# Optimization experiments

Measured on AMD Instinct MI355X. Metric: run time of the kernel, lower is better.

Reference implementation:

```python
import jax, jax.numpy as jnp
import numpy as np

B, S, D, H, L = 16, 1024, 128, 8, 3
DFF = 4 * D  # 512
DH = D // H  # 16
NUM_CLASSES = 6


def layernorm(x, g, b, eps):
    mu = jnp.mean(x, axis=-1, keepdims=True)
    var = jnp.mean(jnp.square(x - mu), axis=-1, keepdims=True)
    return g * (x - mu) / jnp.sqrt(var + eps) + b


def setup_inputs() -> dict:
    key = jax.random.key(0)
    ks = jax.random.split(key, 16)
    sc = 0.05
    inp = {
        'x': jax.random.normal(ks[0], (B, S, D), dtype=jnp.float32),
        'Wq': jax.random.normal(ks[1], (L, D, D), dtype=jnp.float32) * sc,
        'bq': jnp.zeros((L, D), dtype=jnp.float32),
        'Wk': jax.random.normal(ks[2], (L, D, D), dtype=jnp.float32) * sc,
        'bk': jnp.zeros((L, D), dtype=jnp.float32),
        'Wv': jax.random.normal(ks[3], (L, D, D), dtype=jnp.float32) * sc,
        'bv': jnp.zeros((L, D), dtype=jnp.float32),
        'ln1_g': jnp.ones((L, D), dtype=jnp.float32),
        'ln1_b': jnp.zeros((L, D), dtype=jnp.float32),
        'W1': jax.random.normal(ks[4], (L, D, DFF), dtype=jnp.float32) * sc,
        'b1': jnp.zeros((L, DFF), dtype=jnp.float32),
        'W2': jax.random.normal(ks[5], (L, DFF, D), dtype=jnp.float32) * sc,
        'b2': jnp.zeros((L, D), dtype=jnp.float32),
        'ln2_g': jnp.ones((L, D), dtype=jnp.float32),
        'ln2_b': jnp.zeros((L, D), dtype=jnp.float32),
        'Wout': jax.random.normal(ks[6], (D, NUM_CLASSES), dtype=jnp.float32) * sc,
        'bout': jnp.zeros((NUM_CLASSES,), dtype=jnp.float32),
    }
    return inp


def reference(x, Wq, bq, Wk, bk, Wv, bv, ln1_g, ln1_b, W1, b1, W2, b2, ln2_g, ln2_b, Wout, bout):
    scale = 1.0 / jnp.sqrt(jnp.float32(DH))
    for l in range(L):
        # Q/K/V projections with ReLU activation (as in source Dense(..., relu))
        q = jax.nn.relu(jnp.einsum('bsd,de->bse', x, Wq[l]) + bq[l])
        k = jax.nn.relu(jnp.einsum('bsd,de->bse', x, Wk[l]) + bk[l])
        v = jax.nn.relu(jnp.einsum('bsd,de->bse', x, Wv[l]) + bv[l])
        # split-heads (tf.split axis=-1 / concat axis=0 == reshape to heads)
        qh = q.reshape(B, S, H, DH)
        kh = k.reshape(B, S, H, DH)
        vh = v.reshape(B, S, H, DH)
        scores = jnp.einsum('bqhd,bkhd->bhqk', qh, kh) * scale  # [B,H,S,S]
        attn = jax.nn.softmax(scores, axis=-1)
        o = jnp.einsum('bhqk,bkhd->bqhd', attn, vh).reshape(B, S, D)
        x = layernorm(o + x, ln1_g[l], ln1_b[l], 1e-8)
        # pointwise FFN (Conv1D kernel_size=1 == dense over last dim)
        h = jax.nn.relu(jnp.einsum('bsd,df->bsf', x, W1[l]) + b1[l])
        f = jnp.einsum('bsf,fd->bsd', h, W2[l]) + b2[l]
        x = layernorm(f + x, ln2_g[l], ln2_b[l], 1e-6)
    return jnp.einsum('bsd,dc->bsc', x, Wout) + bout
```

## Files before the change

### kernel.cpp

```cpp
#include <hip/hip_runtime.h>
#include <math.h>

#define Bq 16
#define Sq 1024
#define Dq 128
#define Hq 8
#define DHq 16
#define DFFq 512
#define Lq 3
#define NCLS 6
#define NROWS (Bq * Sq)
#define NX ((size_t)NROWS * Dq)

#define QSCL 0.36067376022224085f

typedef __attribute__((ext_vector_type(8))) short    bf16x8;
typedef __attribute__((ext_vector_type(4))) float    f32x4;
typedef __attribute__((ext_vector_type(4))) _Float16 f16x4;
typedef __attribute__((ext_vector_type(8))) _Float16 f16x8;

__device__ inline ushort f32_to_bf16(float f) {
    union { float f; unsigned u; } v; v.f = f;
    unsigned r = v.u + 0x7fffu + ((v.u >> 16) & 1u);
    return (ushort)(r >> 16);
}

__device__ __forceinline__ float exp2_raw(float x) {
    float r;
    asm("v_exp_f32 %0, %1" : "=v"(r) : "v"(x));
    return r;
}

__global__ __launch_bounds__(256) void prep_kernel(
    const float* __restrict__ Wqp, const float* __restrict__ Wkp,
    const float* __restrict__ Wvp, const float* __restrict__ W1p,
    const float* __restrict__ W2p, const float* __restrict__ xp,
    ushort* __restrict__ wbf, ushort* __restrict__ xbf)
{
    const int gid = blockIdx.x * 256 + threadIdx.x;
    if (gid < 147456) {
        const int w   = gid / 49152;
        const int rem = gid - w * 49152;
        const int l   = rem >> 14;
        const int idx = rem & 16383;
        const int k   = idx >> 7;
        const int n   = idx & 127;
        const float* src = (w == 0) ? Wqp : (w == 1) ? Wkp : Wvp;
        const float scl = (w == 0) ? QSCL : 1.0f;
        wbf[(size_t)(w * 3 + l) * 16384 + n * 128 + k] =
            f32_to_bf16(src[(size_t)l * 16384 + k * 128 + n] * scl);
    } else if (gid < 344064) {
        const int g   = gid - 147456;
        const int l   = g >> 16;
        const int idx = g & 65535;
        const int k   = idx >> 9;
        const int n   = idx & 511;
        wbf[147456 + (size_t)l * 65536 + n * 128 + k] =
            f32_to_bf16(W1p[(size_t)l * 65536 + k * 512 + n]);
    } else if (gid < 540672) {
        const int g   = gid - 344064;
        const int l   = g >> 16;
        const int idx = g & 65535;
        const int k   = idx >> 7;
        const int n   = idx & 127;
        wbf[344064 + (size_t)l * 65536 + n * 512 + k] =
            f32_to_bf16(W2p[(size_t)l * 65536 + k * 128 + n]);
    } else {
        const int g = gid - 540672;
        xbf[g] = f32_to_bf16(xp[g]);
    }
}

__global__ __launch_bounds__(256) void gemm_qkv(
    const ushort* __restrict__ A,
    const ushort* __restrict__ wq, const ushort* __restrict__ wk,
    const ushort* __restrict__ wv,
    const float* __restrict__ bqp, const float* __restrict__ bkp,
    const float* __restrict__ bvp,
    _Float16* __restrict__ qo, _Float16* __restrict__ ko,
    _Float16* __restrict__ vo)
{
    __shared__ ushort As[64 * 40];
    __shared__ ushort Bs[128 * 40];

    const int sel  = blockIdx.y;
    const ushort* Bt   = (sel == 0) ? wq : (sel == 1) ? wk : wv;
    const float*  bias = (sel == 0) ? bqp : (sel == 1) ? bkp : bvp;
    const float   bscl = (sel == 0) ? QSCL : 1.0f;

    const int tid  = threadIdx.x;
    const int row0 = blockIdx.x * 64;
    const int wave = tid >> 6;
    const int lane = tid & 63;
    const int quad = lane >> 4;
    const int m16  = lane & 15;
    const int wm   = wave >> 1;
    const int wn   = wave & 1;

    const int sar = tid >> 2;
    const int sac = (tid & 3) * 8;

    f32x4 acc[2][4];
    #pragma unroll
    for (int i = 0; i < 2; ++i)
        #pragma unroll
        for (int j = 0; j < 4; ++j) acc[i][j] = (f32x4)0.f;

    for (int k0 = 0; k0 < 128; k0 += 32) {
        bf16x8 av = *(const bf16x8*)(A + (size_t)(row0 + sar) * 128 + k0 + sac);
        const int r1 = tid >> 2, r2 = r1 + 64;
        bf16x8 bv1 = *(const bf16x8*)(Bt + (size_t)r1 * 128 + k0 + sac);
        bf16x8 bv2 = *(const bf16x8*)(Bt + (size_t)r2 * 128 + k0 + sac);

        __syncthreads();
        *(bf16x8*)&As[sar * 40 + sac] = av;
        *(bf16x8*)&Bs[r1 * 40 + sac]  = bv1;
        *(bf16x8*)&Bs[r2 * 40 + sac]  = bv2;
        __syncthreads();

        bf16x8 af[2], bf[4];
        #pragma unroll
        for (int i = 0; i < 2; ++i)
            af[i] = *(const bf16x8*)&As[(32 * wm + 16 * i + m16) * 40 + quad * 8];
        #pragma unroll
        for (int j = 0; j < 4; ++j)
            bf[j] = *(const bf16x8*)&Bs[(64 * wn + 16 * j + m16) * 40 + quad * 8];
        #pragma unroll
        for (int i = 0; i < 2; ++i)
            #pragma unroll
            for (int j = 0; j < 4; ++j)
                acc[i][j] = __builtin_amdgcn_mfma_f32_16x16x32_bf16(af[i], bf[j], acc[i][j], 0, 0, 0);
    }

    #pragma unroll
    for (int i = 0; i < 2; ++i) {
        #pragma unroll
        for (int j = 0; j < 4; ++j) {
            const int col = 64 * wn + 16 * j + m16;
            const float bb = bias[col] * bscl;
            const int hh = col >> 4, dh = col & 15;
            #pragma unroll
            for (int r = 0; r < 4; ++r) {
                float val = fmaxf(acc[i][j][r] + bb, 0.f);
                const int gr = row0 + 32 * wm + 16 * i + quad * 4 + r;
                const int b = gr >> 10, s = gr & 1023;
                if (sel == 2) {
                    vo[(((size_t)b * Hq + hh) * DHq + dh) * Sq + s] = (_Float16)val;
                } else {
                    _Float16* outp = (sel == 0) ? qo : ko;
                    outp[(((size_t)b * Hq + hh) * Sq + s) * DHq + dh] = (_Float16)val;
                }
            }
        }
    }
}

__global__ __launch_bounds__(256) void gemm_ffn_fused(
    const _Float16* __restrict__ o, const float* __restrict__ resid,
    const float* __restrict__ g1, const float* __restrict__ beta1,
    const ushort* __restrict__ W1t, const float* __restrict__ bias1,
    const ushort* __restrict__ W2t, const float* __restrict__ bias2,
    const float* __restrict__ g2, const float* __restrict__ beta2,
    float* __restrict__ xb,
    const ushort* __restrict__ wqn, const ushort* __restrict__ wkn,
    const ushort* __restrict__ wvn,
    const float* __restrict__ bqn, const float* __restrict__ bkn,
    const float* __restrict__ bvn,
    _Float16* __restrict__ qo, _Float16* __restrict__ ko,
    _Float16* __restrict__ vo, int do_next,
    const float* __restrict__ Wout, const float* __restrict__ bout,
    float* __restrict__ out, int last)
{
    __shared__ __align__(16) char smem[69120];
    ushort*    Af   = (ushort*)smem;
    ushort*    Hs   = (ushort*)(smem + 8704);
    ushort*    Bs   = (ushort*)(smem + 41984);
    float*     wo_s = (float*)(smem + 41984);
    _Float16*  vals = (_Float16*)(smem + 60416);
    float*     mus  = (float*)(smem + 68864);
    float*     rsds = (float*)(smem + 68992);

    const int tid  = threadIdx.x;
    const int row0 = blockIdx.x * 32;
    const int wave = tid >> 6;
    const int lane = tid & 63;
    const int quad = lane >> 4;
    const int m16  = lane & 15;
    const int wm   = wave >> 1;
    const int wn   = wave & 1;
    const int sac  = (tid & 3) * 8;
    const int r1   = tid >> 2, r2 = r1 + 64;

    #pragma unroll 2
    for (int it = 0; it < 8; ++it) {
        const int rr = wave * 8 + it;
        const size_t base = (size_t)(row0 + rr) * Dq;
        float v0 = (float)o[base + lane]      + resid[base + lane];
        float v1 = (float)o[base + 64 + lane] + resid[base + 64 + lane];

        float s = v0 + v1;
        #pragma unroll
        for (int off = 32; off > 0; off >>= 1) s += __shfl_xor(s, off, 64);
        const float mu = s * (1.f / 128.f);
        const float d0 = v0 - mu, d1 = v1 - mu;
        float vs = d0 * d0 + d1 * d1;
        #pragma unroll
        for (int off = 32; off > 0; off >>= 1) vs += __shfl_xor(vs, off, 64);
        const float rstd = rsqrtf(vs * (1.f / 128.f) + 1e-8f);

        const float rv0 = g1[lane]      * d0 * rstd + beta1[lane];
        const float rv1 = g1[lane + 64] * d1 * rstd + beta1[lane + 64];
        Af[rr * 136 + lane]        = f32_to_bf16(rv0);
        Af[rr * 136 + 64 + lane]   = f32_to_bf16(rv1);
        vals[rr * 132 + lane]      = (_Float16)rv0;
        vals[rr * 132 + 64 + lane] = (_Float16)rv1;
    }

    f32x4 acc[4];
    #pragma unroll
    for (int j = 0; j < 4; ++j) acc[j] = (f32x4)0.f;

    for (int idx = 0; idx < 8; ++idx) {
        const int cc = idx >> 1;
        const int k0 = (idx & 1) * 64;

        bf16x8 w11 = *(const bf16x8*)(W1t + (size_t)(cc * 128 + r1) * 128 + k0 + sac);
        bf16x8 w12 = *(const bf16x8*)(W1t + (size_t)(cc * 128 + r1) * 128 + k0 + 32 + sac);
        bf16x8 w21 = *(const bf16x8*)(W1t + (size_t)(cc * 128 + r2) * 128 + k0 + sac);
        bf16x8 w22 = *(const bf16x8*)(W1t + (size_t)(cc * 128 + r2) * 128 + k0 + 32 + sac);

        __syncthreads();
        *(bf16x8*)&Bs[r1 * 72 + sac]      = w11;
        *(bf16x8*)&Bs[r1 * 72 + 32 + sac] = w12;
        *(bf16x8*)&Bs[r2 * 72 + sac]      = w21;
        *(bf16x8*)&Bs[r2 * 72 + 32 + sac] = w22;
        __syncthreads();

        #pragma unroll
        for (int hh = 0; hh < 2; ++hh) {
            const int kk = k0 + hh * 32;
            const bf16x8 af = *(const bf16x8*)&Af[(16 * wm + m16) * 136 + kk + quad * 8];
            bf16x8 bf[4];
            #pragma unroll
            for (int j = 0; j < 4; ++j)
                bf[j] = *(const bf16x8*)&Bs[(64 * wn + 16 * j + m16) * 72 + hh * 32 + quad * 8];
            #pragma unroll
            for (int j = 0; j < 4; ++j)
                acc[j] = __builtin_amdgcn_mfma_f32_16x16x32_bf16(af, bf[j], acc[j], 0, 0, 0);
        }

        if (idx & 1) {
            #pragma unroll
            for (int j = 0; j < 4; ++j) {
                const int col = cc * 128 + 64 * wn + 16 * j + m16;
                const float bb = bias1[col];
                #pragma unroll
                for (int r = 0; r < 4; ++r) {
                    const int row = 16 * wm + quad * 4 + r;
                    Hs[row * 520 + col] = f32_to_bf16(fmaxf(acc[j][r] + bb, 0.f));
                }
                acc[j] = (f32x4)0.f;
            }
        }
    }

    f32x4 acc2[4];
    #pragma unroll
    for (int j = 0; j < 4; ++j) acc2[j] = (f32x4)0.f;

    for (int kc = 0; kc < 8; ++kc) {
        const int k0 = kc * 64;

        bf16x8 w11 = *(const bf16x8*)(W2t + (size_t)r1 * DFFq + k0 + sac);
        bf16x8 w12 = *(const bf16x8*)(W2t + (size_t)r1 * DFFq + k0 + 32 + sac);
        bf16x8 w21 = *(const bf16x8*)(W2t + (size_t)r2 * DFFq + k0 + sac);
        bf16x8 w22 = *(const bf16x8*)(W2t + (size_t)r2 * DFFq + k0 + 32 + sac);

        __syncthreads();
        *(bf16x8*)&Bs[r1 * 72 + sac]      = w11;
        *(bf16x8*)&Bs[r1 * 72 + 32 + sac] = w12;
        *(bf16x8*)&Bs[r2 * 72 + sac]      = w21;
        *(bf16x8*)&Bs[r2 * 72 + 32 + sac] = w22;
        __syncthreads();

        #pragma unroll
        for (int hh = 0; hh < 2; ++hh) {
            const int kk = k0 + hh * 32;
            const bf16x8 af = *(const bf16x8*)&Hs[(16 * wm + m16) * 520 + kk + quad * 8];
            bf16x8 bf[4];
            #pragma unroll
            for (int j = 0; j < 4; ++j)
                bf[j] = *(const bf16x8*)&Bs[(64 * wn + 16 * j + m16) * 72 + hh * 32 + quad * 8];
            #pragma unroll
            for (int j = 0; j < 4; ++j)
                acc2[j] = __builtin_amdgcn_mfma_f32_16x16x32_bf16(af, bf[j], acc2[j], 0, 0, 0);
        }
    }

    __syncthreads();

    float vreg[4][4];
    #pragma unroll
    for (int j = 0; j < 4; ++j) {
        const int col = 64 * wn + 16 * j + m16;
        const float bb = bias2[col];
        #pragma unroll
        for (int r = 0; r < 4; ++r) {
            const int row = 16 * wm + quad * 4 + r;
            float v = acc2[j][r] + bb + (float)vals[row * 132 + col];
            vreg[j][r] = v;
            vals[row * 132 + col] = (_Float16)v;
        }
    }
    if (last) {
        #pragma unroll
        for (int i = 0; i < 3; ++i) wo_s[tid + i * 256] = Wout[tid + i * 256];
    }
    __syncthreads();

    if (tid < 32) {
        float s = 0.f, s2 = 0.f;
        #pragma unroll 8
        for (int c = 0; c < Dq; ++c) {
            float x = (float)vals[tid * 132 + c];
            s += x; s2 = fmaf(x, x, s2);
        }
        const float mu  = s * (1.f / 128.f);
        const float var = s2 * (1.f / 128.f) - mu * mu;
        mus[tid]  = mu;
        rsds[tid] = rsqrtf(var + 1e-6f);
    }
    __syncthreads();

    if (!last) {
        #pragma unroll
        for (int j = 0; j < 4; ++j) {
            const int col = 64 * wn + 16 * j + m16;
            #pragma unroll
            for (int r = 0; r < 4; ++r) {
                const int row = 16 * wm + quad * 4 + r;
                const float rn = g2[col] * (vreg[j][r] - mus[row]) * rsds[row] + beta2[col];
                xb[(size_t)(row0 + row) * Dq + col] = rn;
                Af[row * 136 + col] = f32_to_bf16(rn);
            }
        }

        if (do_next) {
            for (int sel = 0; sel < 3; ++sel) {
                const ushort* Bt   = (sel == 0) ? wqn : (sel == 1) ? wkn : wvn;
                const float*  bias = (sel == 0) ? bqn : (sel == 1) ? bkn : bvn;
                const float   bscl = (sel == 0) ? QSCL : 1.0f;

                f32x4 qacc[4];
                #pragma unroll
                for (int j = 0; j < 4; ++j) qacc[j] = (f32x4)0.f;

                for (int half = 0; half < 2; ++half) {
                    const int k0 = half * 64;
                    bf16x8 w11 = *(const bf16x8*)(Bt + (size_t)r1 * 128 + k0 + sac);
                    bf16x8 w12 = *(const bf16x8*)(Bt + (size_t)r1 * 128 + k0 + 32 + sac);
                    bf16x8 w21 = *(const bf16x8*)(Bt + (size_t)r2 * 128 + k0 + sac);
                    bf16x8 w22 = *(const bf16x8*)(Bt + (size_t)r2 * 128 + k0 + 32 + sac);

                    __syncthreads();
                    *(bf16x8*)&Bs[r1 * 72 + sac]      = w11;
                    *(bf16x8*)&Bs[r1 * 72 + 32 + sac] = w12;
                    *(bf16x8*)&Bs[r2 * 72 + sac]      = w21;
                    *(bf16x8*)&Bs[r2 * 72 + 32 + sac] = w22;
                    __syncthreads();

                    #pragma unroll
                    for (int hh = 0; hh < 2; ++hh) {
                        const int kk = k0 + hh * 32;
                        const bf16x8 af = *(const bf16x8*)&Af[(16 * wm + m16) * 136 + kk + quad * 8];
                        bf16x8 bf[4];
                        #pragma unroll
                        for (int j = 0; j < 4; ++j)
                            bf[j] = *(const bf16x8*)&Bs[(64 * wn + 16 * j + m16) * 72 + hh * 32 + quad * 8];
                        #pragma unroll
                        for (int j = 0; j < 4; ++j)
                            qacc[j] = __builtin_amdgcn_mfma_f32_16x16x32_bf16(af, bf[j], qacc[j], 0, 0, 0);
                    }
                }

                #pragma unroll
                for (int j = 0; j < 4; ++j) {
                    const int col = 64 * wn + 16 * j + m16;
                    const float bb = bias[col] * bscl;
                    const int hh = col >> 4, dh = col & 15;
                    #pragma unroll
                    for (int r = 0; r < 4; ++r) {
                        float val = fmaxf(qacc[j][r] + bb, 0.f);
                        const int gr = row0 + 16 * wm + quad * 4 + r;
                        const int b = gr >> 10, s = gr & 1023;
                        if (sel == 2) {
                            vo[(((size_t)b * Hq + hh) * DHq + dh) * Sq + s] = (_Float16)val;
                        } else {
                            _Float16* outp = (sel == 0) ? qo : ko;
                            outp[(((size_t)b * Hq + hh) * Sq + s) * DHq + dh] = (_Float16)val;
                        }
                    }
                }
            }
        }
    } else {
        #pragma unroll
        for (int j = 0; j < 4; ++j) {
            const int col = 64 * wn + 16 * j + m16;
            #pragma unroll
            for (int r = 0; r < 4; ++r) {
                const int row = 16 * wm + quad * 4 + r;
                vals[row * 132 + col] =
                    (_Float16)(g2[col] * (vreg[j][r] - mus[row]) * rsds[row] + beta2[col]);
            }
        }
        __syncthreads();
        if (tid < 32 * NCLS) {
            const int row = tid / NCLS;
            const int c   = tid - row * NCLS;
            float a = bout[c];
            #pragma unroll 8
            for (int kk = 0; kk < Dq; ++kk)
                a = fmaf((float)vals[row * 132 + kk], wo_s[kk * NCLS + c], a);
            out[(size_t)(row0 + row) * NCLS + c] = a;
        }
    }
}

__global__ __launch_bounds__(256) void attn_mfma(
    const _Float16* __restrict__ q, const _Float16* __restrict__ k,
    const _Float16* __restrict__ vt, _Float16* __restrict__ o)
{
    __shared__ _Float16 Ks[256 * 20];
    __shared__ _Float16 Vs[16 * 264];

    const int bh   = blockIdx.x;
    const int qc   = blockIdx.y;
    const int b    = bh >> 3;
    const int h    = bh & 7;
    const int tid  = threadIdx.x;
    const int wave = tid >> 6;
    const int lane = tid & 63;
    const int quad = lane >> 4;
    const int m16  = lane & 15;
    const int q0   = qc * 128 + wave * 32;

    const f16x4 qf0 = *(const f16x4*)(q + (((size_t)bh * Sq) + q0 + m16) * DHq + quad * 4);
    const f16x4 qf1 = *(const f16x4*)(q + (((size_t)bh * Sq) + q0 + 16 + m16) * DHq + quad * 4);

    const _Float16* kg  = k  + (size_t)bh * Sq * DHq;
    const _Float16* vtg = vt + (size_t)bh * DHq * Sq;

    f32x4 oacc0 = (f32x4)0.f, oacc1 = (f32x4)0.f;
    float lacc0 = 0.f, lacc1 = 0.f;

    const int krow = tid;
    const int vrow = tid >> 4;
    const int vcol = (tid & 15) * 16;

    for (int kb = 0; kb < 4; ++kb) {
        f16x8 ka  = *(const f16x8*)(kg + ((size_t)kb * 256 + krow) * DHq);
        f16x8 kb8 = *(const f16x8*)(kg + ((size_t)kb * 256 + krow) * DHq + 8);
        f16x8 va  = *(const f16x8*)(vtg + (size_t)vrow * Sq + kb * 256 + vcol);
        f16x8 vb  = *(const f16x8*)(vtg + (size_t)vrow * Sq + kb * 256 + vcol + 8);
        __syncthreads();
        *(f16x8*)&Ks[krow * 20 + 0] = ka;
        *(f16x8*)&Ks[krow * 20 + 8] = kb8;
        *(f16x8*)&Vs[vrow * 264 + vcol + 0] = va;
        *(f16x8*)&Vs[vrow * 264 + vcol + 8] = vb;
        __syncthreads();

        #pragma unroll 4
        for (int kt = 0; kt < 16; ++kt) {
            const f16x4 kf = *(const f16x4*)&Ks[(kt * 16 + m16) * 20 + quad * 4];
            const f16x4 vf = *(const f16x4*)&Vs[m16 * 264 + kt * 16 + quad * 4];

            f32x4 st0 = __builtin_amdgcn_mfma_f32_16x16x16f16(kf, qf0, (f32x4)0.f, 0, 0, 0);
            f32x4 st1 = __builtin_amdgcn_mfma_f32_16x16x16f16(kf, qf1, (f32x4)0.f, 0, 0, 0);

            float p00 = exp2_raw(st0[0]);
            float p01 = exp2_raw(st0[1]);
            float p02 = exp2_raw(st0[2]);
            float p03 = exp2_raw(st0[3]);
            float p10 = exp2_raw(st1[0]);
            float p11 = exp2_raw(st1[1]);
            float p12 = exp2_raw(st1[2]);
            float p13 = exp2_raw(st1[3]);
            lacc0 += (p00 + p01) + (p02 + p03);
            lacc1 += (p10 + p11) + (p12 + p13);

            f16x4 pf0, pf1;
            pf0[0] = (_Float16)p00; pf0[1] = (_Float16)p01;
            pf0[2] = (_Float16)p02; pf0[3] = (_Float16)p03;
            pf1[0] = (_Float16)p10; pf1[1] = (_Float16)p11;
            pf1[2] = (_Float16)p12; pf1[3] = (_Float16)p13;

            oacc0 = __builtin_amdgcn_mfma_f32_16x16x16f16(pf0, vf, oacc0, 0, 0, 0);
            oacc1 = __builtin_amdgcn_mfma_f32_16x16x16f16(pf1, vf, oacc1, 0, 0, 0);
        }
    }

    lacc0 += __shfl_xor(lacc0, 16, 64);
    lacc0 += __shfl_xor(lacc0, 32, 64);
    lacc1 += __shfl_xor(lacc1, 16, 64);
    lacc1 += __shfl_xor(lacc1, 32, 64);

    #pragma unroll
    for (int r = 0; r < 4; ++r) {
        const float ls0 = __shfl(lacc0, quad * 4 + r, 64);
        const float ls1 = __shfl(lacc1, quad * 4 + r, 64);
        o[((size_t)b * Sq + q0 + quad * 4 + r) * Dq + h * DHq + m16]      = (_Float16)(oacc0[r] / ls0);
        o[((size_t)b * Sq + q0 + 16 + quad * 4 + r) * Dq + h * DHq + m16] = (_Float16)(oacc1[r] / ls1);
    }
}

extern "C" void kernel_launch(void* const* d_in, const int* in_sizes, int n_in,
                              void* d_out, int out_size, void* d_ws, size_t ws_size,
                              hipStream_t stream)
{
    const float* x_in  = (const float*)d_in[0];
    const float* Wq    = (const float*)d_in[1];
    const float* bq    = (const float*)d_in[2];
    const float* Wk    = (const float*)d_in[3];
    const float* bk    = (const float*)d_in[4];
    const float* Wv    = (const float*)d_in[5];
    const float* bv    = (const float*)d_in[6];
    const float* ln1_g = (const float*)d_in[7];
    const float* ln1_b = (const float*)d_in[8];
    const float* W1    = (const float*)d_in[9];
    const float* b1    = (const float*)d_in[10];
    const float* W2    = (const float*)d_in[11];
    const float* b2    = (const float*)d_in[12];
    const float* ln2_g = (const float*)d_in[13];
    const float* ln2_b = (const float*)d_in[14];
    const float* Wout  = (const float*)d_in[15];
    const float* bout  = (const float*)d_in[16];
    float* out = (float*)d_out;

    float* ws = (float*)d_ws;
    _Float16* qf16 = (_Float16*)ws;
    _Float16* kf16 = (_Float16*)(ws + NX / 2);
    _Float16* vt16 = (_Float16*)(ws + NX);
    float*    xb   = ws + 9 * NX / 2;
    ushort*   xbf0 = (ushort*)(ws + 11 * NX / 2);
    ushort*   wbf  = (ushort*)(ws + 7 * NX);
    _Float16* obuf = (_Float16*)(ws + 8 * NX);

    prep_kernel<<<dim3(10304), dim3(256), 0, stream>>>(Wq, Wk, Wv, W1, W2, x_in, wbf, xbf0);

    const dim3 blk(256);

    {
        const ushort* wqt = wbf + (size_t)0 * 16384;
        const ushort* wkt = wbf + (size_t)3 * 16384;
        const ushort* wvt = wbf + (size_t)6 * 16384;
        gemm_qkv<<<dim3(256, 3), blk, 0, stream>>>(
            xbf0, wqt, wkt, wvt, bq, bk, bv, qf16, kf16, vt16);
    }

    const float* xcur = x_in;
    for (int l = 0; l < Lq; ++l) {
        const ushort* w1t = wbf + 147456 + (size_t)l * 65536;
        const ushort* w2t = wbf + 344064 + (size_t)l * 65536;
        const int next = (l < Lq - 1) ? 1 : 0;
        const int ln   = l + 1;
        const ushort* wqn = next ? (wbf + (size_t)(0 * 3 + ln) * 16384) : wbf;
        const ushort* wkn = next ? (wbf + (size_t)(1 * 3 + ln) * 16384) : wbf;
        const ushort* wvn = next ? (wbf + (size_t)(2 * 3 + ln) * 16384) : wbf;
        const float*  bqn = next ? (bq + ln * Dq) : bq;
        const float*  bkn = next ? (bk + ln * Dq) : bk;
        const float*  bvn = next ? (bv + ln * Dq) : bv;

        attn_mfma<<<dim3(Bq * Hq, 8), blk, 0, stream>>>(qf16, kf16, vt16, obuf);

        gemm_ffn_fused<<<dim3(512), blk, 0, stream>>>(
            obuf, xcur, ln1_g + l * Dq, ln1_b + l * Dq,
            w1t, b1 + l * DFFq, w2t, b2 + l * Dq,
            ln2_g + l * Dq, ln2_b + l * Dq,
            xb,
            wqn, wkn, wvn, bqn, bkn, bvn,
            qf16, kf16, vt16, next,
            Wout, bout, out, (l == Lq - 1) ? 1 : 0);

        xcur = xb;
    }
}
```

Before: 254.8 us.

## Prefetch next weight/KV tiles into registers and vectorize LN and softmax epilogue

Across the GEMM, FFN, QKV and attention kernels, each loop now issues the next tile's global loads into registers right after the LDS store barrier, so memory latency overlaps with the MFMA work on the current tile. The layernorm loads and stores become paired vector accesses. The second layernorm's row statistics are split over all 256 threads with shuffle reductions instead of a serial 32-thread loop. The attention epilogue uses packed fp16 conversion (round toward zero) and a fast reciprocal instead of division, which slightly changes rounding, and the register prefetch raises register pressure.

```diff
diff --git a/kernel.cpp b/kernel.cpp
--- a/kernel.cpp
+++ b/kernel.cpp
@@ -18,6 +18,7 @@
 typedef __attribute__((ext_vector_type(4))) float    f32x4;
 typedef __attribute__((ext_vector_type(4))) _Float16 f16x4;
 typedef __attribute__((ext_vector_type(8))) _Float16 f16x8;
+typedef __attribute__((ext_vector_type(2))) _Float16 f16x2;
 
 __device__ inline ushort f32_to_bf16(float f) {
     union { float f; unsigned u; } v; v.f = f;
@@ -29,6 +30,16 @@
     float r;
     asm("v_exp_f32 %0, %1" : "=v"(r) : "v"(x));
     return r;
+}
+
+__device__ __forceinline__ float rcp_fast(float x) {
+    float r;
+    asm("v_rcp_f32 %0, %1" : "=v"(r) : "v"(x));
+    return r;
+}
+
+__device__ __forceinline__ f16x2 pkrtz(float a, float b) {
+    return __builtin_bit_cast(f16x2, __builtin_amdgcn_cvt_pkrtz(a, b));
 }
 
 __global__ __launch_bounds__(256) void prep_kernel(
@@ -106,17 +117,24 @@
         #pragma unroll
         for (int j = 0; j < 4; ++j) acc[i][j] = (f32x4)0.f;
 
+    const int r1 = tid >> 2, r2 = r1 + 64;
+
+    bf16x8 av  = *(const bf16x8*)(A  + (size_t)(row0 + sar) * 128 + sac);
+    bf16x8 bv1 = *(const bf16x8*)(Bt + (size_t)r1 * 128 + sac);
+    bf16x8 bv2 = *(const bf16x8*)(Bt + (size_t)r2 * 128 + sac);
+
     for (int k0 = 0; k0 < 128; k0 += 32) {
-        bf16x8 av = *(const bf16x8*)(A + (size_t)(row0 + sar) * 128 + k0 + sac);
-        const int r1 = tid >> 2, r2 = r1 + 64;
-        bf16x8 bv1 = *(const bf16x8*)(Bt + (size_t)r1 * 128 + k0 + sac);
-        bf16x8 bv2 = *(const bf16x8*)(Bt + (size_t)r2 * 128 + k0 + sac);
-
         __syncthreads();
         *(bf16x8*)&As[sar * 40 + sac] = av;
         *(bf16x8*)&Bs[r1 * 40 + sac]  = bv1;
         *(bf16x8*)&Bs[r2 * 40 + sac]  = bv2;
         __syncthreads();
+
+        if (k0 < 96) {
+            av  = *(const bf16x8*)(A  + (size_t)(row0 + sar) * 128 + k0 + 32 + sac);
+            bv1 = *(const bf16x8*)(Bt + (size_t)r1 * 128 + k0 + 32 + sac);
+            bv2 = *(const bf16x8*)(Bt + (size_t)r2 * 128 + k0 + 32 + sac);
+        }
 
         bf16x8 af[2], bf[4];
         #pragma unroll
@@ -191,12 +209,17 @@
     const int sac  = (tid & 3) * 8;
     const int r1   = tid >> 2, r2 = r1 + 64;
 
+    const int ca = lane * 2;
+    const float2 gg  = *(const float2*)(g1 + ca);
+    const float2 bt1 = *(const float2*)(beta1 + ca);
     #pragma unroll 2
     for (int it = 0; it < 8; ++it) {
         const int rr = wave * 8 + it;
         const size_t base = (size_t)(row0 + rr) * Dq;
-        float v0 = (float)o[base + lane]      + resid[base + lane];
-        float v1 = (float)o[base + 64 + lane] + resid[base + 64 + lane];
+        const f16x2  ov = *(const f16x2*)(o + base + ca);
+        const float2 rv = *(const float2*)(resid + base + ca);
+        const float v0 = (float)ov[0] + rv.x;
+        const float v1 = (float)ov[1] + rv.y;
 
         float s = v0 + v1;
         #pragma unroll
@@ -208,26 +231,26 @@
         for (int off = 32; off > 0; off >>= 1) vs += __shfl_xor(vs, off, 64);
         const float rstd = rsqrtf(vs * (1.f / 128.f) + 1e-8f);
 
-        const float rv0 = g1[lane]      * d0 * rstd + beta1[lane];
-        const float rv1 = g1[lane + 64] * d1 * rstd + beta1[lane + 64];
-        Af[rr * 136 + lane]        = f32_to_bf16(rv0);
-        Af[rr * 136 + 64 + lane]   = f32_to_bf16(rv1);
-        vals[rr * 132 + lane]      = (_Float16)rv0;
-        vals[rr * 132 + 64 + lane] = (_Float16)rv1;
+        const float rv0 = gg.x * d0 * rstd + bt1.x;
+        const float rv1 = gg.y * d1 * rstd + bt1.y;
+        ushort2 ab; ab.x = f32_to_bf16(rv0); ab.y = f32_to_bf16(rv1);
+        *(ushort2*)&Af[rr * 136 + ca] = ab;
+        f16x2 vv; vv[0] = (_Float16)rv0; vv[1] = (_Float16)rv1;
+        *(f16x2*)&vals[rr * 132 + ca] = vv;
     }
 
     f32x4 acc[4];
     #pragma unroll
     for (int j = 0; j < 4; ++j) acc[j] = (f32x4)0.f;
 
+    bf16x8 w11 = *(const bf16x8*)(W1t + (size_t)r1 * 128 + sac);
+    bf16x8 w12 = *(const bf16x8*)(W1t + (size_t)r1 * 128 + 32 + sac);
+    bf16x8 w21 = *(const bf16x8*)(W1t + (size_t)r2 * 128 + sac);
+    bf16x8 w22 = *(const bf16x8*)(W1t + (size_t)r2 * 128 + 32 + sac);
+
     for (int idx = 0; idx < 8; ++idx) {
         const int cc = idx >> 1;
         const int k0 = (idx & 1) * 64;
-
-        bf16x8 w11 = *(const bf16x8*)(W1t + (size_t)(cc * 128 + r1) * 128 + k0 + sac);
-        bf16x8 w12 = *(const bf16x8*)(W1t + (size_t)(cc * 128 + r1) * 128 + k0 + 32 + sac);
-        bf16x8 w21 = *(const bf16x8*)(W1t + (size_t)(cc * 128 + r2) * 128 + k0 + sac);
-        bf16x8 w22 = *(const bf16x8*)(W1t + (size_t)(cc * 128 + r2) * 128 + k0 + 32 + sac);
 
         __syncthreads();
         *(bf16x8*)&Bs[r1 * 72 + sac]      = w11;
@@ -235,6 +258,15 @@
         *(bf16x8*)&Bs[r2 * 72 + sac]      = w21;
         *(bf16x8*)&Bs[r2 * 72 + 32 + sac] = w22;
         __syncthreads();
+
+        if (idx < 7) {
+            const int cc2 = (idx + 1) >> 1;
+            const int k02 = ((idx + 1) & 1) * 64;
+            w11 = *(const bf16x8*)(W1t + (size_t)(cc2 * 128 + r1) * 128 + k02 + sac);
+            w12 = *(const bf16x8*)(W1t + (size_t)(cc2 * 128 + r1) * 128 + k02 + 32 + sac);
+            w21 = *(const bf16x8*)(W1t + (size_t)(cc2 * 128 + r2) * 128 + k02 + sac);
+            w22 = *(const bf16x8*)(W1t + (size_t)(cc2 * 128 + r2) * 128 + k02 + 32 + sac);
+        }
 
         #pragma unroll
         for (int hh = 0; hh < 2; ++hh) {
@@ -268,13 +300,13 @@
     #pragma unroll
     for (int j = 0; j < 4; ++j) acc2[j] = (f32x4)0.f;
 
+    w11 = *(const bf16x8*)(W2t + (size_t)r1 * DFFq + sac);
+    w12 = *(const bf16x8*)(W2t + (size_t)r1 * DFFq + 32 + sac);
+    w21 = *(const bf16x8*)(W2t + (size_t)r2 * DFFq + sac);
+    w22 = *(const bf16x8*)(W2t + (size_t)r2 * DFFq + 32 + sac);
+
     for (int kc = 0; kc < 8; ++kc) {
         const int k0 = kc * 64;
-
-        bf16x8 w11 = *(const bf16x8*)(W2t + (size_t)r1 * DFFq + k0 + sac);
-        bf16x8 w12 = *(const bf16x8*)(W2t + (size_t)r1 * DFFq + k0 + 32 + sac);
-        bf16x8 w21 = *(const bf16x8*)(W2t + (size_t)r2 * DFFq + k0 + sac);
-        bf16x8 w22 = *(const bf16x8*)(W2t + (size_t)r2 * DFFq + k0 + 32 + sac);
 
         __syncthreads();
         *(bf16x8*)&Bs[r1 * 72 + sac]      = w11;
@@ -282,6 +314,14 @@
         *(bf16x8*)&Bs[r2 * 72 + sac]      = w21;
         *(bf16x8*)&Bs[r2 * 72 + 32 + sac] = w22;
         __syncthreads();
+
+        if (kc < 7) {
+            const int k02 = (kc + 1) * 64;
+            w11 = *(const bf16x8*)(W2t + (size_t)r1 * DFFq + k02 + sac);
+            w12 = *(const bf16x8*)(W2t + (size_t)r1 * DFFq + k02 + 32 + sac);
+            w21 = *(const bf16x8*)(W2t + (size_t)r2 * DFFq + k02 + sac);
+            w22 = *(const bf16x8*)(W2t + (size_t)r2 * DFFq + k02 + 32 + sac);
+        }
 
         #pragma unroll
         for (int hh = 0; hh < 2; ++hh) {
@@ -318,17 +358,27 @@
     }
     __syncthreads();
 
-    if (tid < 32) {
+    {
+        const int row = tid >> 3;
+        const int c0  = (tid & 7) * 16;
         float s = 0.f, s2 = 0.f;
-        #pragma unroll 8
-        for (int c = 0; c < Dq; ++c) {
-            float x = (float)vals[tid * 132 + c];
-            s += x; s2 = fmaf(x, x, s2);
-        }
-        const float mu  = s * (1.f / 128.f);
-        const float var = s2 * (1.f / 128.f) - mu * mu;
-        mus[tid]  = mu;
-        rsds[tid] = rsqrtf(var + 1e-6f);
+        #pragma unroll
+        for (int u = 0; u < 4; ++u) {
+            const f16x4 xv = *(const f16x4*)&vals[row * 132 + c0 + u * 4];
+            #pragma unroll
+            for (int e = 0; e < 4; ++e) {
+                const float x = (float)xv[e];
+                s += x; s2 = fmaf(x, x, s2);
+            }
+        }
+        s  += __shfl_xor(s, 1, 64);  s  += __shfl_xor(s, 2, 64);  s  += __shfl_xor(s, 4, 64);
+        s2 += __shfl_xor(s2, 1, 64); s2 += __shfl_xor(s2, 2, 64); s2 += __shfl_xor(s2, 4, 64);
+        if ((tid & 7) == 0) {
+            const float mu  = s * (1.f / 128.f);
+            const float var = s2 * (1.f / 128.f) - mu * mu;
+            mus[row]  = mu;
+            rsds[row] = rsqrtf(var + 1e-6f);
+        }
     }
     __syncthreads();
 
@@ -346,58 +396,70 @@
         }
 
         if (do_next) {
-            for (int sel = 0; sel < 3; ++sel) {
-                const ushort* Bt   = (sel == 0) ? wqn : (sel == 1) ? wkn : wvn;
-                const float*  bias = (sel == 0) ? bqn : (sel == 1) ? bkn : bvn;
-                const float   bscl = (sel == 0) ? QSCL : 1.0f;
-
-                f32x4 qacc[4];
+            bf16x8 q11 = *(const bf16x8*)(wqn + (size_t)r1 * 128 + sac);
+            bf16x8 q12 = *(const bf16x8*)(wqn + (size_t)r1 * 128 + 32 + sac);
+            bf16x8 q21 = *(const bf16x8*)(wqn + (size_t)r2 * 128 + sac);
+            bf16x8 q22 = *(const bf16x8*)(wqn + (size_t)r2 * 128 + 32 + sac);
+
+            f32x4 qacc[4];
+            for (int st = 0; st < 6; ++st) {
+                const int sel  = st >> 1;
+                const int half = st & 1;
+                if (half == 0) {
+                    #pragma unroll
+                    for (int j = 0; j < 4; ++j) qacc[j] = (f32x4)0.f;
+                }
+
+                __syncthreads();
+                *(bf16x8*)&Bs[r1 * 72 + sac]      = q11;
+                *(bf16x8*)&Bs[r1 * 72 + 32 + sac] = q12;
+                *(bf16x8*)&Bs[r2 * 72 + sac]      = q21;
+                *(bf16x8*)&Bs[r2 * 72 + 32 + sac] = q22;
+                __syncthreads();
+
+                if (st < 5) {
+                    const int sel2 = (st + 1) >> 1;
+                    const int k02  = ((st + 1) & 1) * 64;
+                    const ushort* Bt2 = (sel2 == 0) ? wqn : (sel2 == 1) ? wkn : wvn;
+                    q11 = *(const bf16x8*)(Bt2 + (size_t)r1 * 128 + k02 + sac);
+                    q12 = *(const bf16x8*)(Bt2 + (size_t)r1 * 128 + k02 + 32 + sac);
+                    q21 = *(const bf16x8*)(Bt2 + (size_t)r2 * 128 + k02 + sac);
+                    q22 = *(const bf16x8*)(Bt2 + (size_t)r2 * 128 + k02 + 32 + sac);
+                }
+
+                const int k0 = half * 64;
                 #pragma unroll
-                for (int j = 0; j < 4; ++j) qacc[j] = (f32x4)0.f;
-
-                for (int half = 0; half < 2; ++half) {
-                    const int k0 = half * 64;
-                    bf16x8 w11 = *(const bf16x8*)(Bt + (size_t)r1 * 128 + k0 + sac);
-                    bf16x8 w12 = *(const bf16x8*)(Bt + (size_t)r1 * 128 + k0 + 32 + sac);
-                    bf16x8 w21 = *(const bf16x8*)(Bt + (size_t)r2 * 128 + k0 + sac);
-                    bf16x8 w22 = *(const bf16x8*)(Bt + (size_t)r2 * 128 + k0 + 32 + sac);
-
-                    __syncthreads();
-                    *(bf16x8*)&Bs[r1 * 72 + sac]      = w11;
-                    *(bf16x8*)&Bs[r1 * 72 + 32 + sac] = w12;
-                    *(bf16x8*)&Bs[r2 * 72 + sac]      = w21;
-                    *(bf16x8*)&Bs[r2 * 72 + 32 + sac] = w22;
-                    __syncthreads();
-
+                for (int hh = 0; hh < 2; ++hh) {
+                    const int kk = k0 + hh * 32;
+                    const bf16x8 af = *(const bf16x8*)&Af[(16 * wm + m16) * 136 + kk + quad * 8];
+                    bf16x8 bf[4];
                     #pragma unroll
-                    for (int hh = 0; hh < 2; ++hh) {
-                        const int kk = k0 + hh * 32;
-                        const bf16x8 af = *(const bf16x8*)&Af[(16 * wm + m16) * 136 + kk + quad * 8];
-                        bf16x8 bf[4];
+                    for (int j = 0; j < 4; ++j)
+                        bf[j] = *(const bf16x8*)&Bs[(64 * wn + 16 * j + m16) * 72 + hh * 32 + quad * 8];
+                    #pragma unroll
+                    for (int j = 0; j < 4; ++j)
+                        qacc[j] = __builtin_amdgcn_mfma_f32_16x16x32_bf16(af, bf[j], qacc[j], 0, 0, 0);
+                }
+
+                if (half) {
+                    const float* bias = (sel == 0) ? bqn : (sel == 1) ? bkn : bvn;
+                    const float  bscl = (sel == 0) ? QSCL : 1.0f;
+                    #pragma unroll
+                    for (int j = 0; j < 4; ++j) {
+                        const int col = 64 * wn + 16 * j + m16;
+                        const float bb = bias[col] * bscl;
+                        const int hh = col >> 4, dh = col & 15;
                         #pragma unroll
-                        for (int j = 0; j < 4; ++j)
-                            bf[j] = *(const bf16x8*)&Bs[(64 * wn + 16 * j + m16) * 72 + hh * 32 + quad * 8];
-                        #pragma unroll
-                        for (int j = 0; j < 4; ++j)
-                            qacc[j] = __builtin_amdgcn_mfma_f32_16x16x32_bf16(af, bf[j], qacc[j], 0, 0, 0);
-                    }
-                }
-
-                #pragma unroll
-                for (int j = 0; j < 4; ++j) {
-                    const int col = 64 * wn + 16 * j + m16;
-                    const float bb = bias[col] * bscl;
-                    const int hh = col >> 4, dh = col & 15;
-                    #pragma unroll
-                    for (int r = 0; r < 4; ++r) {
-                        float val = fmaxf(qacc[j][r] + bb, 0.f);
-                        const int gr = row0 + 16 * wm + quad * 4 + r;
-                        const int b = gr >> 10, s = gr & 1023;
-                        if (sel == 2) {
-                            vo[(((size_t)b * Hq + hh) * DHq + dh) * Sq + s] = (_Float16)val;
-                        } else {
-                            _Float16* outp = (sel == 0) ? qo : ko;
-                            outp[(((size_t)b * Hq + hh) * Sq + s) * DHq + dh] = (_Float16)val;
+                        for (int r = 0; r < 4; ++r) {
+                            float val = fmaxf(qacc[j][r] + bb, 0.f);
+                            const int gr = row0 + 16 * wm + quad * 4 + r;
+                            const int b = gr >> 10, s = gr & 1023;
+                            if (sel == 2) {
+                                vo[(((size_t)b * Hq + hh) * DHq + dh) * Sq + s] = (_Float16)val;
+                            } else {
+                                _Float16* outp = (sel == 0) ? qo : ko;
+                                outp[(((size_t)b * Hq + hh) * Sq + s) * DHq + dh] = (_Float16)val;
+                            }
                         }
                     }
                 }
@@ -458,11 +520,12 @@
     const int vrow = tid >> 4;
     const int vcol = (tid & 15) * 16;
 
+    f16x8 ka  = *(const f16x8*)(kg + (size_t)krow * DHq);
+    f16x8 kb8 = *(const f16x8*)(kg + (size_t)krow * DHq + 8);
+    f16x8 va  = *(const f16x8*)(vtg + (size_t)vrow * Sq + vcol);
+    f16x8 vb  = *(const f16x8*)(vtg + (size_t)vrow * Sq + vcol + 8);
+
     for (int kb = 0; kb < 4; ++kb) {
-        f16x8 ka  = *(const f16x8*)(kg + ((size_t)kb * 256 + krow) * DHq);
-        f16x8 kb8 = *(const f16x8*)(kg + ((size_t)kb * 256 + krow) * DHq + 8);
-        f16x8 va  = *(const f16x8*)(vtg + (size_t)vrow * Sq + kb * 256 + vcol);
-        f16x8 vb  = *(const f16x8*)(vtg + (size_t)vrow * Sq + kb * 256 + vcol + 8);
         __syncthreads();
         *(f16x8*)&Ks[krow * 20 + 0] = ka;
         *(f16x8*)&Ks[krow * 20 + 8] = kb8;
@@ -470,6 +533,15 @@
         *(f16x8*)&Vs[vrow * 264 + vcol + 8] = vb;
         __syncthreads();
 
+        if (kb < 3) {
+            const _Float16* kp = kg  + ((size_t)(kb + 1) * 256 + krow) * DHq;
+            const _Float16* vp = vtg + (size_t)vrow * Sq + (kb + 1) * 256 + vcol;
+            ka  = *(const f16x8*)(kp);
+            kb8 = *(const f16x8*)(kp + 8);
+            va  = *(const f16x8*)(vp);
+            vb  = *(const f16x8*)(vp + 8);
+        }
+
         #pragma unroll 4
         for (int kt = 0; kt < 16; ++kt) {
             const f16x4 kf = *(const f16x4*)&Ks[(kt * 16 + m16) * 20 + quad * 4];
@@ -478,22 +550,25 @@
             f32x4 st0 = __builtin_amdgcn_mfma_f32_16x16x16f16(kf, qf0, (f32x4)0.f, 0, 0, 0);
             f32x4 st1 = __builtin_amdgcn_mfma_f32_16x16x16f16(kf, qf1, (f32x4)0.f, 0, 0, 0);
 
-            float p00 = exp2_raw(st0[0]);
-            float p01 = exp2_raw(st0[1]);
-            float p02 = exp2_raw(st0[2]);
-            float p03 = exp2_raw(st0[3]);
-            float p10 = exp2_raw(st1[0]);
-            float p11 = exp2_raw(st1[1]);
-            float p12 = exp2_raw(st1[2]);
-            float p13 = exp2_raw(st1[3]);
+            const float p00 = exp2_raw(st0[0]);
+            const float p01 = exp2_raw(st0[1]);
+            const float p02 = exp2_raw(st0[2]);
+            const float p03 = exp2_raw(st0[3]);
+            const float p10 = exp2_raw(st1[0]);
+            const float p11 = exp2_raw(st1[1]);
+            const float p12 = exp2_raw(st1[2]);
+            const float p13 = exp2_raw(st1[3]);
+
             lacc0 += (p00 + p01) + (p02 + p03);
             lacc1 += (p10 + p11) + (p12 + p13);
 
-            f16x4 pf0, pf1;
-            pf0[0] = (_Float16)p00; pf0[1] = (_Float16)p01;
-            pf0[2] = (_Float16)p02; pf0[3] = (_Float16)p03;
-            pf1[0] = (_Float16)p10; pf1[1] = (_Float16)p11;
-            pf1[2] = (_Float16)p12; pf1[3] = (_Float16)p13;
+            const f16x2 a0 = pkrtz(p00, p01);
+            const f16x2 a1 = pkrtz(p02, p03);
+            const f16x2 b0 = pkrtz(p10, p11);
+            const f16x2 b1 = pkrtz(p12, p13);
+
+            const f16x4 pf0 = __builtin_shufflevector(a0, a1, 0, 1, 2, 3);
+            const f16x4 pf1 = __builtin_shufflevector(b0, b1, 0, 1, 2, 3);
 
             oacc0 = __builtin_amdgcn_mfma_f32_16x16x16f16(pf0, vf, oacc0, 0, 0, 0);
             oacc1 = __builtin_amdgcn_mfma_f32_16x16x16f16(pf1, vf, oacc1, 0, 0, 0);
@@ -505,12 +580,15 @@
     lacc1 += __shfl_xor(lacc1, 16, 64);
     lacc1 += __shfl_xor(lacc1, 32, 64);
 
+    const float linv0 = rcp_fast(lacc0);
+    const float linv1 = rcp_fast(lacc1);
+
     #pragma unroll
     for (int r = 0; r < 4; ++r) {
-        const float ls0 = __shfl(lacc0, quad * 4 + r, 64);
-        const float ls1 = __shfl(lacc1, quad * 4 + r, 64);
-        o[((size_t)b * Sq + q0 + quad * 4 + r) * Dq + h * DHq + m16]      = (_Float16)(oacc0[r] / ls0);
-        o[((size_t)b * Sq + q0 + 16 + quad * 4 + r) * Dq + h * DHq + m16] = (_Float16)(oacc1[r] / ls1);
+        const float i0 = __shfl(linv0, quad * 4 + r, 64);
+        const float i1 = __shfl(linv1, quad * 4 + r, 64);
+        o[((size_t)b * Sq + q0 + quad * 4 + r) * Dq + h * DHq + m16]      = (_Float16)(oacc0[r] * i0);
+        o[((size_t)b * Sq + q0 + 16 + quad * 4 + r) * Dq + h * DHq + m16] = (_Float16)(oacc1[r] * i1);
     }
 }
 
```

Measured after the change: 248.5 us. 1.03x faster.
